# Kernel tuning notes

Hardware: AMD Instinct MI355X
Metric: run time of the kernel (lower is better)

Reference implementation:

```python
import jax, jax.numpy as jnp
import numpy as np

N = 100_000   # nodes
E = 1_600_000 # edges (avg degree 16)
D = 128       # feature dim (input = hidden = output = mlp hidden)
L = 3         # GIN layers
EPS = 0.0     # init_eps, not learned


def setup_inputs() -> dict:
    key = jax.random.key(0)
    ks = jax.random.split(key, 7)
    feat = jax.random.normal(ks[0], (N, D), jnp.float32)
    # scale weights ~ 1/sqrt(fan_in) for numerically sane activations
    W1 = jax.random.normal(ks[1], (L, D, D), jnp.float32) / np.float32(np.sqrt(D))
    b1 = jax.random.normal(ks[2], (L, D), jnp.float32) * 0.01
    W2 = jax.random.normal(ks[3], (L, D, D), jnp.float32) / np.float32(np.sqrt(D))
    b2 = jax.random.normal(ks[4], (L, D), jnp.float32) * 0.01
    src = jax.random.randint(ks[5], (E,), 0, N, dtype=jnp.int32)
    dst = jax.random.randint(ks[6], (E,), 0, N, dtype=jnp.int32)
    return {"feat": feat, "W1": W1, "b1": b1, "W2": W2, "b2": b2,
            "src": src, "dst": dst}


def reference(feat, W1, b1, W2, b2, src, dst):
    h = feat
    for i in range(L):
        # sum-aggregate neighbor (source) features into destination nodes
        neigh = jax.ops.segment_sum(h[src], dst, num_segments=N)  # [N, D]
        rst = (1.0 + EPS) * h + neigh
        # 2-layer MLP: hidden layer uses act+norm(none), last layer is plain linear
        if i < L - 1:
            h1 = jax.nn.relu(rst @ W1[i] + b1[i])
            h2 = h1 @ W2[i] + b2[i]
            h = jax.nn.relu(h2)  # ApplyNodeFunc: norm(none) -> relu
        else:
            # last GIN layer: activation 'none' everywhere
            h1 = rst @ W1[i] + b1[i]
            h = h1 @ W2[i] + b2[i]
    return h
```

## Files before the change

### kernel.cpp

```cpp
#include <hip/hip_runtime.h>
#include <hip/hip_bf16.h>

#define D 128
#define NBUCK_SHIFT 9

typedef __bf16 bf16x8 __attribute__((ext_vector_type(8)));
typedef float f32x4 __attribute__((ext_vector_type(4)));
typedef unsigned int u32x4 __attribute__((ext_vector_type(4)));
typedef unsigned short u16x4_t __attribute__((ext_vector_type(4)));
typedef unsigned short u16x8_t __attribute__((ext_vector_type(8)));

__device__ __forceinline__ float b2f(unsigned short u) {
    unsigned int x = ((unsigned int)u) << 16;
    return __builtin_bit_cast(float, x);
}
__device__ __forceinline__ unsigned short f2b(float f) {
    __hip_bfloat16 h = __float2bfloat16(f);
    return __builtin_bit_cast(unsigned short, h);
}

__device__ __forceinline__ void acc8(float* acc, u32x4 x) {
#pragma unroll
    for (int r = 0; r < 4; ++r) {
        acc[2 * r]     += __builtin_bit_cast(float, x[r] << 16);
        acc[2 * r + 1] += __builtin_bit_cast(float, x[r] & 0xffff0000u);
    }
}

__global__ __launch_bounds__(256) void coarse_hist_kernel(
        const int* __restrict__ dst, int* __restrict__ bco, int E, int nbuck) {
    __shared__ int s[256];
    int t = threadIdx.x;
    s[t] = 0;
    __syncthreads();
    for (int i = blockIdx.x * 256 + t; i < E; i += gridDim.x * 256)
        atomicAdd(&s[dst[i] >> NBUCK_SHIFT], 1);
    __syncthreads();
    if (t < nbuck && s[t] > 0) atomicAdd(&bco[t], s[t]);
}

__global__ __launch_bounds__(256) void bucket_scan_kernel(
        const int* __restrict__ bco, int* __restrict__ bbase, int nbuck, int E) {
    __shared__ int s[256];
    int t = threadIdx.x;
    int c = (t < nbuck) ? bco[t] : 0;
    s[t] = c;
    __syncthreads();
    for (int o = 1; o < 256; o <<= 1) {
        int y = (t >= o) ? s[t - o] : 0;
        __syncthreads();
        s[t] += y;
        __syncthreads();
    }
    if (t < nbuck) bbase[t] = s[t] - c;
    if (t == 0) bbase[nbuck] = E;
}

__global__ __launch_bounds__(256) void bucket_kernel(
        const int* __restrict__ src, const int* __restrict__ dst,
        const int* __restrict__ bbase, int* __restrict__ bcursor,
        int2* __restrict__ pairs, int E, int nbuck) {
    __shared__ int lcnt[256];
    __shared__ int lbase[256];
    int t = threadIdx.x;
    int base = blockIdx.x * 4096;
    if (t < nbuck) lcnt[t] = 0;
    __syncthreads();
    int d[16], s[16];
#pragma unroll
    for (int k = 0; k < 16; ++k) {
        int i = base + t + k * 256;
        if (i < E) {
            d[k] = dst[i];
            s[k] = src[i];
            atomicAdd(&lcnt[d[k] >> NBUCK_SHIFT], 1);
        } else {
            d[k] = -1;
            s[k] = 0;
        }
    }
    __syncthreads();
    if (t < nbuck) {
        int c = lcnt[t];
        int g = (c > 0) ? atomicAdd(&bcursor[t], c) : 0;
        lbase[t] = bbase[t] + g;
        lcnt[t] = 0;
    }
    __syncthreads();
#pragma unroll
    for (int k = 0; k < 16; ++k) {
        if (d[k] >= 0) {
            int b = d[k] >> NBUCK_SHIFT;
            int r = atomicAdd(&lcnt[b], 1);
            pairs[lbase[b] + r] = make_int2(s[k], d[k]);
        }
    }
}

__global__ __launch_bounds__(1024) void bucket_build_kernel(
        const int2* __restrict__ pairs, const int* __restrict__ bbase,
        int* __restrict__ row_ptr, int* __restrict__ col, int N, int E) {
    __shared__ int cnt[512];
    __shared__ int off[512];
    int t = threadIdx.x;
    int b = blockIdx.x;
    int s0 = bbase[b], s1 = bbase[b + 1];
    if (t < 512) cnt[t] = 0;
    __syncthreads();
    for (int i = s0 + t; i < s1; i += 1024)
        atomicAdd(&cnt[pairs[i].y & 511], 1);
    __syncthreads();
    int c = (t < 512) ? cnt[t] : 0;
    if (t < 512) off[t] = c;
    __syncthreads();
    for (int o = 1; o < 512; o <<= 1) {
        int y = (t < 512 && t >= o) ? off[t - o] : 0;
        __syncthreads();
        if (t < 512) off[t] += y;
        __syncthreads();
    }
    int v0 = b << NBUCK_SHIFT;
    if (t < 512) {
        int ex = off[t] - c;
        off[t] = ex;
        cnt[t] = 0;
        if (v0 + t < N) row_ptr[v0 + t] = s0 + ex;
    }
    __syncthreads();
    for (int i = s0 + t; i < s1; i += 1024) {
        int2 p = pairs[i];
        int li = p.y & 511;
        int slot = s0 + off[li] + atomicAdd(&cnt[li], 1);
        col[slot] = p.x;
    }
    if (b == 0 && t == 0) row_ptr[N] = E;
}

__global__ void f32_to_bf16_kernel(const float4* __restrict__ in, ushort4* __restrict__ out, int n4) {
    int i = blockIdx.x * blockDim.x + threadIdx.x;
    if (i < n4) {
        float4 f = in[i];
        ushort4 o;
        o.x = f2b(f.x); o.y = f2b(f.y); o.z = f2b(f.z); o.w = f2b(f.w);
        out[i] = o;
    }
}

__global__ void wtrans_kernel(const float* __restrict__ W1, const float* __restrict__ W2,
                              unsigned short* __restrict__ W1L, unsigned short* __restrict__ W2L,
                              int total) {
    int i = blockIdx.x * blockDim.x + threadIdx.x;
    if (i < total) {
        int l = i >> 14;
        int rem = i & 16383;
        int k = rem >> 7;
        int n = rem & 127;
        int nt = n >> 4, l15 = n & 15;
        int kb = k >> 5, lg = (k >> 3) & 3, j = k & 7;
        int o = ((l * 32 + nt * 4 + kb) * 64 + lg * 16 + l15) * 8 + j;
        W1L[o] = f2b(W1[i]);
        W2L[o] = f2b(W2[i]);
    }
}

__global__ __launch_bounds__(256) void agg_kernel(
        const unsigned short* __restrict__ h, const int* __restrict__ row_ptr,
        const int* __restrict__ col, unsigned short* __restrict__ rst, int N) {
    int lane = threadIdx.x & 63;
    int i = lane & 15;
    int j = lane >> 4;
    int v = blockIdx.x * 4 + (threadIdx.x >> 6);
    if (v >= N) return;

    const unsigned short* hb = h + i * 8;
    int e0 = row_ptr[v], e1 = row_ptr[v + 1];

    float accA[8], accB[8], accC[8], accD[8];
#pragma unroll
    for (int r = 0; r < 8; ++r) { accA[r] = 0.f; accB[r] = 0.f; accC[r] = 0.f; accD[r] = 0.f; }

    if (j == 0) {
        u32x4 x = *(const u32x4*)(hb + (size_t)v * D);
        acc8(accA, x);
    }

    int e = e0 + j;
    for (; e + 12 < e1; e += 16) {
        int u0 = col[e];
        int u1 = col[e + 4];
        int u2 = col[e + 8];
        int u3 = col[e + 12];
        u32x4 x0 = *(const u32x4*)(hb + (size_t)u0 * D);
        u32x4 x1 = *(const u32x4*)(hb + (size_t)u1 * D);
        u32x4 x2 = *(const u32x4*)(hb + (size_t)u2 * D);
        u32x4 x3 = *(const u32x4*)(hb + (size_t)u3 * D);
        acc8(accA, x0);
        acc8(accB, x1);
        acc8(accC, x2);
        acc8(accD, x3);
    }
    for (; e + 4 < e1; e += 8) {
        int u0 = col[e];
        int u1 = col[e + 4];
        u32x4 x0 = *(const u32x4*)(hb + (size_t)u0 * D);
        u32x4 x1 = *(const u32x4*)(hb + (size_t)u1 * D);
        acc8(accA, x0);
        acc8(accB, x1);
    }
    if (e < e1) {
        u32x4 x0 = *(const u32x4*)(hb + (size_t)col[e] * D);
        acc8(accA, x0);
    }

    unsigned short outv[8];
#pragma unroll
    for (int r = 0; r < 8; ++r) {
        float s = (accA[r] + accB[r]) + (accC[r] + accD[r]);
        s += __shfl_xor(s, 16);
        s += __shfl_xor(s, 32);
        outv[r] = f2b(s);
    }
    if (j == 0) {
        u16x8_t o;
#pragma unroll
        for (int r = 0; r < 8; ++r) o[r] = outv[r];
        *(u16x8_t*)(rst + (size_t)v * D + i * 8) = o;
    }
}

__global__ __launch_bounds__(256, 4) void mlp_kernel(
        const unsigned short* __restrict__ A, const unsigned short* __restrict__ W1L,
        const unsigned short* __restrict__ W2L, const float* __restrict__ b1,
        const float* __restrict__ b2, unsigned short* __restrict__ hOut,
        float* __restrict__ fOut, int mode, int ntiles, int N) {
    __shared__ float b1s[128], b2s[128];
    __shared__ unsigned short tilebuf[4 * 2560];
    int tid = threadIdx.x;
    if (tid < 128) b1s[tid] = b1[tid];
    else b2s[tid - 128] = b2[tid - 128];
    __syncthreads();
    int wave = tid >> 6, lane = tid & 63, l15 = lane & 15, lg = lane >> 4;
    unsigned short* buf = tilebuf + wave * 2560;
    int tile = blockIdx.x * 4 + wave;
    if (tile >= ntiles) return;
    int v0 = tile << 4;

    bf16x8 bfrag[4];
    const unsigned short* arow = A + (size_t)(v0 + l15) * D + lg * 8;
#pragma unroll
    for (int kb = 0; kb < 4; ++kb) bfrag[kb] = *(const bf16x8*)(arow + kb * 32);

    f32x4 acc[8];
#pragma unroll
    for (int nt = 0; nt < 8; ++nt) acc[nt] = (f32x4){0.f, 0.f, 0.f, 0.f};
#pragma unroll
    for (int kb = 0; kb < 4; ++kb)
#pragma unroll
        for (int nt = 0; nt < 8; ++nt) {
            bf16x8 wf = *(const bf16x8*)(W1L + ((nt * 4 + kb) * 64 + lane) * 8);
            acc[nt] = __builtin_amdgcn_mfma_f32_16x16x32_bf16(wf, bfrag[kb], acc[nt], 0, 0, 0);
        }
#pragma unroll
    for (int nt = 0; nt < 8; ++nt) {
        f32x4 bias = *(const f32x4*)(b1s + nt * 16 + lg * 4);
        int kb2 = nt >> 1;
        int lgk = (nt & 1) * 2 + (lg >> 1);
        int U = kb2 * 80 + l15 * 5 + lgk;
        u16x4_t o;
#pragma unroll
        for (int r = 0; r < 4; ++r) {
            float x = acc[nt][r] + bias[r];
            if (mode == 0) x = fmaxf(x, 0.f);
            o[r] = f2b(x);
        }
        *(u16x4_t*)(buf + U * 8 + (lg & 1) * 4) = o;
    }
    bf16x8 bf2[4];
#pragma unroll
    for (int kb = 0; kb < 4; ++kb)
        bf2[kb] = *(const bf16x8*)(buf + (kb * 80 + l15 * 5 + lg) * 8);
#pragma unroll
    for (int nt = 0; nt < 8; ++nt) acc[nt] = (f32x4){0.f, 0.f, 0.f, 0.f};
#pragma unroll
    for (int kb = 0; kb < 4; ++kb)
#pragma unroll
        for (int nt = 0; nt < 8; ++nt) {
            bf16x8 wf = *(const bf16x8*)(W2L + ((nt * 4 + kb) * 64 + lane) * 8);
            acc[nt] = __builtin_amdgcn_mfma_f32_16x16x32_bf16(wf, bf2[kb], acc[nt], 0, 0, 0);
        }
    int m = v0 + l15;
    if (m < N) {
#pragma unroll
        for (int nt = 0; nt < 8; ++nt) {
            f32x4 bias = *(const f32x4*)(b2s + nt * 16 + lg * 4);
            int c0 = nt * 16 + lg * 4;
            if (mode == 0) {
                u16x4_t o;
#pragma unroll
                for (int r = 0; r < 4; ++r) o[r] = f2b(fmaxf(acc[nt][r] + bias[r], 0.f));
                *(u16x4_t*)(hOut + (size_t)m * D + c0) = o;
            } else {
                f32x4 o;
#pragma unroll
                for (int r = 0; r < 4; ++r) o[r] = acc[nt][r] + bias[r];
                *(f32x4*)(fOut + (size_t)m * D + c0) = o;
            }
        }
    }
}

extern "C" void kernel_launch(void* const* d_in, const int* in_sizes, int n_in,
                              void* d_out, int out_size, void* d_ws, size_t ws_size,
                              hipStream_t stream) {
    const float* feat = (const float*)d_in[0];
    const float* W1 = (const float*)d_in[1];
    const float* b1 = (const float*)d_in[2];
    const float* W2 = (const float*)d_in[3];
    const float* b2 = (const float*)d_in[4];
    const int* src = (const int*)d_in[5];
    const int* dst = (const int*)d_in[6];

    const int N = in_sizes[0] / D;
    const int L = in_sizes[2] / D;
    const int E = in_sizes[5];

    char* w = (char*)d_ws;
    size_t off = 0;
    auto alloc = [&](size_t bytes) {
        void* p = w + off;
        off = (off + bytes + 255) & ~(size_t)255;
        return p;
    };
    unsigned short* bufA = (unsigned short*)alloc((size_t)N * D * 2);
    unsigned short* bufB = (unsigned short*)alloc((size_t)N * D * 2);
    size_t unionBytes = (size_t)N * D * 2;
    if ((size_t)E * 8 > unionBytes) unionBytes = (size_t)E * 8;
    unsigned short* bufR = (unsigned short*)alloc(unionBytes);
    int2* pairs = (int2*)bufR;
    int* col = (int*)alloc((size_t)E * 4);
    int* row_ptr = (int*)alloc((size_t)(N + 1) * 4);
    int* bco = (int*)alloc(512 * 4);
    int* bcursor = bco + 256;
    int* bbase = (int*)alloc(257 * 4);
    unsigned short* W1L = (unsigned short*)alloc((size_t)L * 16384 * 2);
    unsigned short* W2L = (unsigned short*)alloc((size_t)L * 16384 * 2);

    int nbuck = (N + (1 << NBUCK_SHIFT) - 1) >> NBUCK_SHIFT;

    hipMemsetAsync(bco, 0, 512 * 4, stream);
    coarse_hist_kernel<<<512, 256, 0, stream>>>(dst, bco, E, nbuck);
    bucket_scan_kernel<<<1, 256, 0, stream>>>(bco, bbase, nbuck, E);
    bucket_kernel<<<(E + 4095) / 4096, 256, 0, stream>>>(src, dst, bbase, bcursor, pairs, E, nbuck);
    bucket_build_kernel<<<nbuck, 1024, 0, stream>>>(pairs, bbase, row_ptr, col, N, E);

    int n4 = N * D / 4;
    f32_to_bf16_kernel<<<(n4 + 255) / 256, 256, 0, stream>>>((const float4*)feat, (ushort4*)bufA, n4);
    int wtotal = L * D * D;
    wtrans_kernel<<<(wtotal + 255) / 256, 256, 0, stream>>>(W1, W2, W1L, W2L, wtotal);

    int ntiles = (N + 15) / 16;
    int aggBlocks = (N + 3) / 4;
    int mlpGrid = (ntiles + 3) / 4;
    const unsigned short* hin[3] = {bufA, bufB, bufA};
    unsigned short* hout[3] = {bufB, bufA, nullptr};
    for (int i = 0; i < L; ++i) {
        int mode = (i == L - 1) ? 1 : 0;
        agg_kernel<<<aggBlocks, 256, 0, stream>>>(hin[i], row_ptr, col, bufR, N);
        mlp_kernel<<<mlpGrid, 256, 0, stream>>>(bufR, W1L + (size_t)i * 16384, W2L + (size_t)i * 16384,
                                                b1 + i * D, b2 + i * D, hout[i], (float*)d_out,
                                                mode, ntiles, N);
    }
}
```

Measured before the change: 444.3 us.

## Pad CSR rows to multiples of four with zero-node sentinel for vector index loads

Rebuilds the CSR so each row is padded to a multiple of four entries, with padding pointing at an extra all-zero node row. Column indices are stored pre-scaled to byte offsets, and row bounds are stored as start/end pairs. This lets the aggregation load four neighbour indices with one int4 load, prefetch the next group, and drop the remainder loops. Accumulation uses packed float2 adds. The cost is extra gathers of the zero row, since each row does up to three padded loads, plus a larger index buffer. The 32-bit byte offsets rely on the feature buffer staying under 4 GB.

Measured after the change: 441.0 us. About the same (-0.8%).

```diff
diff --git a/kernel.cpp b/kernel.cpp
--- a/kernel.cpp
+++ b/kernel.cpp
@@ -3,9 +3,11 @@
 
 #define D 128
 #define NBUCK_SHIFT 9
+#define PAD_SLACK 2048
 
 typedef __bf16 bf16x8 __attribute__((ext_vector_type(8)));
 typedef float f32x4 __attribute__((ext_vector_type(4)));
+typedef float f32x2 __attribute__((ext_vector_type(2)));
 typedef unsigned int u32x4 __attribute__((ext_vector_type(4)));
 typedef unsigned short u16x4_t __attribute__((ext_vector_type(4)));
 typedef unsigned short u16x8_t __attribute__((ext_vector_type(8)));
@@ -19,11 +21,13 @@
     return __builtin_bit_cast(unsigned short, h);
 }
 
-__device__ __forceinline__ void acc8(float* acc, u32x4 x) {
+__device__ __forceinline__ void acc8(f32x2* acc, u32x4 x) {
 #pragma unroll
     for (int r = 0; r < 4; ++r) {
-        acc[2 * r]     += __builtin_bit_cast(float, x[r] << 16);
-        acc[2 * r + 1] += __builtin_bit_cast(float, x[r] & 0xffff0000u);
+        f32x2 t;
+        t[0] = __builtin_bit_cast(float, x[r] << 16);
+        t[1] = __builtin_bit_cast(float, x[r] & 0xffff0000u);
+        acc[r] += t;
     }
 }
 
@@ -99,19 +103,21 @@
 
 __global__ __launch_bounds__(1024) void bucket_build_kernel(
         const int2* __restrict__ pairs, const int* __restrict__ bbase,
-        int* __restrict__ row_ptr, int* __restrict__ col, int N, int E) {
+        int2* __restrict__ rowse, int* __restrict__ col, int N, int E) {
     __shared__ int cnt[512];
     __shared__ int off[512];
     int t = threadIdx.x;
     int b = blockIdx.x;
     int s0 = bbase[b], s1 = bbase[b + 1];
+    int p0 = ((s0 + 3) & ~3) + b * PAD_SLACK;
     if (t < 512) cnt[t] = 0;
     __syncthreads();
     for (int i = s0 + t; i < s1; i += 1024)
         atomicAdd(&cnt[pairs[i].y & 511], 1);
     __syncthreads();
     int c = (t < 512) ? cnt[t] : 0;
-    if (t < 512) off[t] = c;
+    int cp = (c + 3) & ~3;
+    if (t < 512) off[t] = cp;
     __syncthreads();
     for (int o = 1; o < 512; o <<= 1) {
         int y = (t < 512 && t >= o) ? off[t - o] : 0;
@@ -121,19 +127,25 @@
     }
     int v0 = b << NBUCK_SHIFT;
     if (t < 512) {
-        int ex = off[t] - c;
+        int ex = off[t] - cp;
         off[t] = ex;
         cnt[t] = 0;
-        if (v0 + t < N) row_ptr[v0 + t] = s0 + ex;
+        if (v0 + t < N) rowse[v0 + t] = make_int2(p0 + ex, p0 + ex + cp);
     }
     __syncthreads();
     for (int i = s0 + t; i < s1; i += 1024) {
         int2 p = pairs[i];
         int li = p.y & 511;
-        int slot = s0 + off[li] + atomicAdd(&cnt[li], 1);
-        col[slot] = p.x;
-    }
-    if (b == 0 && t == 0) row_ptr[N] = E;
+        int slot = p0 + off[li] + atomicAdd(&cnt[li], 1);
+        col[slot] = p.x << 8;
+    }
+    __syncthreads();
+    if (t < 512) {
+        int cc = cnt[t];
+        int base2 = p0 + off[t];
+        int endp = base2 + ((cc + 3) & ~3);
+        for (int q = base2 + cc; q < endp; ++q) col[q] = N << 8;
+    }
 }
 
 __global__ void f32_to_bf16_kernel(const float4* __restrict__ in, ushort4* __restrict__ out, int n4) {
@@ -164,7 +176,7 @@
 }
 
 __global__ __launch_bounds__(256) void agg_kernel(
-        const unsigned short* __restrict__ h, const int* __restrict__ row_ptr,
+        const unsigned short* __restrict__ h, const int2* __restrict__ rowse,
         const int* __restrict__ col, unsigned short* __restrict__ rst, int N) {
     int lane = threadIdx.x & 63;
     int i = lane & 15;
@@ -172,53 +184,58 @@
     int v = blockIdx.x * 4 + (threadIdx.x >> 6);
     if (v >= N) return;
 
-    const unsigned short* hb = h + i * 8;
-    int e0 = row_ptr[v], e1 = row_ptr[v + 1];
-
-    float accA[8], accB[8], accC[8], accD[8];
-#pragma unroll
-    for (int r = 0; r < 8; ++r) { accA[r] = 0.f; accB[r] = 0.f; accC[r] = 0.f; accD[r] = 0.f; }
+    const char* __restrict__ hb = (const char*)h;
+    unsigned ioff = (unsigned)i * 16u;
+    int2 se = rowse[v];
+    int e = se.x + 4 * j;
+    int e1 = se.y;
+
+    f32x2 accA[4], accB[4], accC[4], accD[4];
+#pragma unroll
+    for (int r = 0; r < 4; ++r) {
+        accA[r] = (f32x2){0.f, 0.f};
+        accB[r] = (f32x2){0.f, 0.f};
+        accC[r] = (f32x2){0.f, 0.f};
+        accD[r] = (f32x2){0.f, 0.f};
+    }
 
     if (j == 0) {
-        u32x4 x = *(const u32x4*)(hb + (size_t)v * D);
+        u32x4 x = *(const u32x4*)(hb + (((unsigned)v << 8) + ioff));
         acc8(accA, x);
     }
 
-    int e = e0 + j;
-    for (; e + 12 < e1; e += 16) {
-        int u0 = col[e];
-        int u1 = col[e + 4];
-        int u2 = col[e + 8];
-        int u3 = col[e + 12];
-        u32x4 x0 = *(const u32x4*)(hb + (size_t)u0 * D);
-        u32x4 x1 = *(const u32x4*)(hb + (size_t)u1 * D);
-        u32x4 x2 = *(const u32x4*)(hb + (size_t)u2 * D);
-        u32x4 x3 = *(const u32x4*)(hb + (size_t)u3 * D);
+    bool have = (e < e1);
+    int4 c4;
+    if (have) c4 = *(const int4*)(col + e);
+    while (have) {
+        int en = e + 16;
+        bool haven = (en < e1);
+        int4 c4n;
+        if (haven) c4n = *(const int4*)(col + en);
+        u32x4 x0 = *(const u32x4*)(hb + ((unsigned)c4.x + ioff));
+        u32x4 x1 = *(const u32x4*)(hb + ((unsigned)c4.y + ioff));
+        u32x4 x2 = *(const u32x4*)(hb + ((unsigned)c4.z + ioff));
+        u32x4 x3 = *(const u32x4*)(hb + ((unsigned)c4.w + ioff));
         acc8(accA, x0);
         acc8(accB, x1);
         acc8(accC, x2);
         acc8(accD, x3);
-    }
-    for (; e + 4 < e1; e += 8) {
-        int u0 = col[e];
-        int u1 = col[e + 4];
-        u32x4 x0 = *(const u32x4*)(hb + (size_t)u0 * D);
-        u32x4 x1 = *(const u32x4*)(hb + (size_t)u1 * D);
-        acc8(accA, x0);
-        acc8(accB, x1);
-    }
-    if (e < e1) {
-        u32x4 x0 = *(const u32x4*)(hb + (size_t)col[e] * D);
-        acc8(accA, x0);
+        c4 = c4n;
+        e = en;
+        have = haven;
     }
 
     unsigned short outv[8];
 #pragma unroll
-    for (int r = 0; r < 8; ++r) {
-        float s = (accA[r] + accB[r]) + (accC[r] + accD[r]);
-        s += __shfl_xor(s, 16);
-        s += __shfl_xor(s, 32);
-        outv[r] = f2b(s);
+    for (int r = 0; r < 4; ++r) {
+        f32x2 s = (accA[r] + accB[r]) + (accC[r] + accD[r]);
+        float lo = s[0], hi = s[1];
+        lo += __shfl_xor(lo, 16);
+        lo += __shfl_xor(lo, 32);
+        hi += __shfl_xor(hi, 16);
+        hi += __shfl_xor(hi, 32);
+        outv[2 * r] = f2b(lo);
+        outv[2 * r + 1] = f2b(hi);
     }
     if (j == 0) {
         u16x8_t o;
@@ -331,14 +348,14 @@
         off = (off + bytes + 255) & ~(size_t)255;
         return p;
     };
-    unsigned short* bufA = (unsigned short*)alloc((size_t)N * D * 2);
-    unsigned short* bufB = (unsigned short*)alloc((size_t)N * D * 2);
-    size_t unionBytes = (size_t)N * D * 2;
+    unsigned short* bufA = (unsigned short*)alloc((size_t)(N + 1) * D * 2);
+    unsigned short* bufB = (unsigned short*)alloc((size_t)(N + 1) * D * 2);
+    size_t unionBytes = (size_t)(N + 16) * D * 2;
     if ((size_t)E * 8 > unionBytes) unionBytes = (size_t)E * 8;
     unsigned short* bufR = (unsigned short*)alloc(unionBytes);
     int2* pairs = (int2*)bufR;
-    int* col = (int*)alloc((size_t)E * 4);
-    int* row_ptr = (int*)alloc((size_t)(N + 1) * 4);
+    int* col = (int*)alloc(((size_t)E + 256 * PAD_SLACK + 16) * 4);
+    int2* rowse = (int2*)alloc((size_t)N * 8);
     int* bco = (int*)alloc(512 * 4);
     int* bcursor = bco + 256;
     int* bbase = (int*)alloc(257 * 4);
@@ -348,10 +365,12 @@
     int nbuck = (N + (1 << NBUCK_SHIFT) - 1) >> NBUCK_SHIFT;
 
     hipMemsetAsync(bco, 0, 512 * 4, stream);
+    hipMemsetAsync(bufA + (size_t)N * D, 0, D * 2, stream);
+    hipMemsetAsync(bufB + (size_t)N * D, 0, D * 2, stream);
     coarse_hist_kernel<<<512, 256, 0, stream>>>(dst, bco, E, nbuck);
     bucket_scan_kernel<<<1, 256, 0, stream>>>(bco, bbase, nbuck, E);
     bucket_kernel<<<(E + 4095) / 4096, 256, 0, stream>>>(src, dst, bbase, bcursor, pairs, E, nbuck);
-    bucket_build_kernel<<<nbuck, 1024, 0, stream>>>(pairs, bbase, row_ptr, col, N, E);
+    bucket_build_kernel<<<nbuck, 1024, 0, stream>>>(pairs, bbase, rowse, col, N, E);
 
     int n4 = N * D / 4;
     f32_to_bf16_kernel<<<(n4 + 255) / 256, 256, 0, stream>>>((const float4*)feat, (ushort4*)bufA, n4);
@@ -365,7 +384,7 @@
     unsigned short* hout[3] = {bufB, bufA, nullptr};
     for (int i = 0; i < L; ++i) {
         int mode = (i == L - 1) ? 1 : 0;
-        agg_kernel<<<aggBlocks, 256, 0, stream>>>(hin[i], row_ptr, col, bufR, N);
+        agg_kernel<<<aggBlocks, 256, 0, stream>>>(hin[i], rowse, col, bufR, N);
         mlp_kernel<<<mlpGrid, 256, 0, stream>>>(bufR, W1L + (size_t)i * 16384, W2L + (size_t)i * 16384,
                                                 b1 + i * D, b2 + i * D, hout[i], (float*)d_out,
                                                 mode, ntiles, N);
```
